# Performance work log

Hardware: AMD Instinct MI355X
Metric: run time of the kernel (lower is better)

## Reference

```python
import jax, jax.numpy as jnp
import numpy as np

DIM = 2048
STATE = 2048
SEL_H = 1024
B = 16384


def setup_inputs() -> dict:
    key = jax.random.key(0)
    ks = jax.random.split(key, 7)
    def lin(k, out_f, in_f):
        return jax.random.normal(k, (out_f, in_f), dtype=jnp.float32) / np.sqrt(in_f)
    return {
        "x_t": jax.random.normal(ks[0], (B, DIM), dtype=jnp.float32),
        "h_prev": jax.random.normal(ks[1], (B, STATE), dtype=jnp.float32),
        "W_in": lin(ks[2], STATE, DIM),
        "W_sel_in": lin(ks[3], SEL_H, DIM),
        "W_sel_out": lin(ks[4], 4 * STATE, SEL_H),
        "W_out": lin(ks[5], DIM, STATE),
        "d": jnp.ones((STATE,), dtype=jnp.float32),
    }


def reference(x_t, h_prev, W_in, W_sel_in, W_sel_out, W_out, d):
    # u_t = in_proj(x_t): [B, state]
    u_t = x_t @ W_in.T
    # selector: silu(x @ W_sel_in.T) @ W_sel_out.T -> [B, 4*state]
    sel_h = jax.nn.silu(x_t @ W_sel_in.T)
    sel = sel_h @ W_sel_out.T
    a_raw, b_raw, c_raw, d_raw = jnp.split(sel, 4, axis=-1)
    a_t = jax.nn.sigmoid(a_raw)
    b_t = jnp.tanh(b_raw)
    c_t = jnp.tanh(c_raw)
    d_t = jax.nn.sigmoid(d_raw)
    h_t = a_t * h_prev + b_t * u_t
    y_t = c_t * h_t + d[None, :] * d_t * u_t
    out = y_t @ W_out.T  # [B, dim]
    return (out, h_t)
```

## Files before the change

### kernel.cpp

```cpp
#include <hip/hip_runtime.h>
#include <hip/hip_bf16.h>
#include <cstdint>

#define NB    16384
#define DIMX  2048
#define STATE 2048
#define SELH  1024

typedef unsigned short u16;
typedef short  short8_t __attribute__((ext_vector_type(8)));
typedef float  f32x4    __attribute__((ext_vector_type(4)));

__device__ __forceinline__ u16 f2bf(float f) {
  unsigned u = __builtin_bit_cast(unsigned, f);
  u += 0x7fffu + ((u >> 16) & 1u);
  return (u16)(u >> 16);
}
__device__ __forceinline__ float bf2f(u16 h) {
  unsigned u = ((unsigned)h) << 16;
  return __builtin_bit_cast(float, u);
}
__device__ __forceinline__ float sigmoidf_(float x) { return 1.f / (1.f + __expf(-x)); }
__device__ __forceinline__ float tanhf_(float x)    { return 2.f / (1.f + __expf(-2.f * x)) - 1.f; }

__device__ __forceinline__ f32x4 mfma_bf16(short8_t a, short8_t b, f32x4 c) {
  return __builtin_amdgcn_mfma_f32_16x16x32_bf16(a, b, c, 0, 0, 0);
}

__device__ __forceinline__ void gload16(const void* g, const void* l) {
  __builtin_amdgcn_global_load_lds(
      (const __attribute__((address_space(1))) unsigned int*)(uintptr_t)g,
      (__attribute__((address_space(3))) unsigned int*)(unsigned int)(uintptr_t)l,
      16, 0, 0);
}

#define LDS_V(p) (*(const short8_t*)__builtin_assume_aligned((const void*)(p), 16))

__global__ __launch_bounds__(256) void k_f32_to_bf16(const float* __restrict__ src,
                                                     u16* __restrict__ dst, int n4) {
  int i = blockIdx.x * blockDim.x + threadIdx.x;
  int stride = gridDim.x * blockDim.x;
  for (; i < n4; i += stride) {
    float4 v = ((const float4*)src)[i];
    ushort4 o;
    o.x = f2bf(v.x); o.y = f2bf(v.y); o.z = f2bf(v.z); o.w = f2bf(v.w);
    ((ushort4*)dst)[i] = o;
  }
}

template <int EPI, int KD, int NCOLS>
__global__ __launch_bounds__(512, 2) void k_gemm256(const u16* __restrict__ A,
                                                    const u16* __restrict__ Bsrc,
                                                    float* __restrict__ f32out,
                                                    u16* __restrict__ bfout,
                                                    const float* __restrict__ hprev,
                                                    const u16* __restrict__ ubf,
                                                    const float* __restrict__ dvec) {
  __shared__ __align__(16) char smem[131072];
  const int tid = threadIdx.x;
  const int w = tid >> 6, l = tid & 63;
  const int wr = w >> 2, wc = w & 3;
  const int bx = blockIdx.x, by = blockIdx.y;
  const int m0 = by * 256;

  const unsigned aAddr0 = (unsigned)(wr * 16384 + (l & 15) * 128 +
                                     (((l >> 4) * 16) ^ ((l & 7) << 4)));
  const unsigned aAddr1 = aAddr0 ^ 64u;
  const unsigned bAddr0 = (unsigned)(65536 + (wc * 64 + (l & 15)) * 64 +
                                     (((l >> 4) * 16) ^ ((l & 3) << 4)));
  const unsigned bAddr1 = bAddr0 + 16384u;

  const int rA = tid >> 3;
  const int kA = ((tid & 7) ^ ((tid >> 3) & 7)) * 8;
  const u16* aSrc = A + (size_t)(m0 + rA) * KD + kA;

  const int rB = tid >> 2;
  const int kB = ((tid & 3) ^ ((tid >> 2) & 3)) * 8;
  size_t bRow0, bRow1;
  if constexpr (EPI <= 2) {
    bRow0 = (size_t)bx * 256 + rB;
    bRow1 = bRow0 + 128;
  } else {
    const int s0 = bx * 64;
    const int r1 = rB + 128;
    bRow0 = (size_t)((rB >> 4) & 3) * STATE + s0 + (rB >> 6) * 16 + (rB & 15);
    bRow1 = (size_t)((r1 >> 4) & 3) * STATE + s0 + (r1 >> 6) * 16 + (r1 & 15);
  }
  const u16* bSrc0 = Bsrc + bRow0 * KD + kB;
  const u16* bSrc1 = Bsrc + bRow1 * KD + kB;

  auto stageA = [&](int k0n, int rh, unsigned dstD) {
    const u16* sp = aSrc + (size_t)rh * 128 * KD + k0n;
    gload16(sp,           smem + dstD + (unsigned)rh * 16384u + (unsigned)tid * 16u);
    gload16(sp + 64 * KD, smem + dstD + (unsigned)rh * 16384u + 8192u + (unsigned)tid * 16u);
  };
  auto stageB = [&](int k0n, int kh, unsigned dstD) {
    const int kk = k0n + kh * 32;
    gload16(bSrc0 + kk, smem + 65536u + dstD + (unsigned)kh * 16384u + (unsigned)tid * 16u);
    gload16(bSrc1 + kk, smem + 65536u + dstD + (unsigned)kh * 16384u + 8192u + (unsigned)tid * 16u);
  };

  f32x4 acc[8][4];
#pragma unroll
  for (int i = 0; i < 8; ++i)
#pragma unroll
    for (int j = 0; j < 4; ++j) acc[i][j] = f32x4{0.f, 0.f, 0.f, 0.f};

  short8_t avq[4], bk0[4], bk1[4];

#define PH_TAIL()                                                              \
    __builtin_amdgcn_s_barrier();                                              \
    asm volatile("s_waitcnt lgkmcnt(0)" ::: "memory");                         \
    __builtin_amdgcn_sched_barrier(0);

#define MFMA16(MBASE, BK)                                                      \
    __builtin_amdgcn_s_setprio(1);                                             \
    _Pragma("unroll") for (int mf = 0; mf < 4; ++mf)                           \
      _Pragma("unroll") for (int nf = 0; nf < 4; ++nf)                         \
        acc[(MBASE) + mf][nf] = mfma_bf16(avq[mf], BK[nf],                     \
                                          acc[(MBASE) + mf][nf]);              \
    __builtin_amdgcn_s_setprio(0);                                             \
    __builtin_amdgcn_s_barrier();

#define KTILE(D, DO_STAGE, K0N, LASTT)                                         \
  {                                                                            \
                                                   \
    _Pragma("unroll") for (int mf = 0; mf < 4; ++mf)                           \
        avq[mf] = LDS_V(smem + aAddr0 + (D) * 32768u + mf * 2048u);            \
    _Pragma("unroll") for (int nf = 0; nf < 4; ++nf)                           \
        bk0[nf] = LDS_V(smem + bAddr0 + (D) * 32768u + nf * 1024u);            \
    if (DO_STAGE) stageA(K0N, 0, (D ^ 1) * 32768u);                            \
    PH_TAIL();                                                                 \
    MFMA16(0, bk0);                                                            \
                                                   \
    _Pragma("unroll") for (int mf = 0; mf < 4; ++mf)                           \
        avq[mf] = LDS_V(smem + aAddr0 + (D) * 32768u + (mf + 4) * 2048u);      \
    if (DO_STAGE) stageA(K0N, 1, (D ^ 1) * 32768u);                            \
    if (LASTT) { asm volatile("s_waitcnt vmcnt(0)" ::: "memory"); }            \
    else       { asm volatile("s_waitcnt vmcnt(4)" ::: "memory"); }            \
    PH_TAIL();                                                                 \
    MFMA16(4, bk0);                                                            \
                                                   \
    _Pragma("unroll") for (int mf = 0; mf < 4; ++mf)                           \
        avq[mf] = LDS_V(smem + aAddr1 + (D) * 32768u + mf * 2048u);            \
    _Pragma("unroll") for (int nf = 0; nf < 4; ++nf)                           \
        bk1[nf] = LDS_V(smem + bAddr1 + (D) * 32768u + nf * 1024u);            \
    if (DO_STAGE) stageB(K0N, 0, (D ^ 1) * 32768u);                            \
    PH_TAIL();                                                                 \
    MFMA16(0, bk1);                                                            \
                                                   \
    _Pragma("unroll") for (int mf = 0; mf < 4; ++mf)                           \
        avq[mf] = LDS_V(smem + aAddr1 + (D) * 32768u + (mf + 4) * 2048u);      \
    if (DO_STAGE) stageB(K0N, 1, (D ^ 1) * 32768u);                            \
    if (!LASTT) { asm volatile("s_waitcnt vmcnt(2)" ::: "memory"); }           \
    PH_TAIL();                                                                 \
    MFMA16(4, bk1);                                                            \
  }

  stageA(0, 0, 0u); stageA(0, 1, 0u); stageB(0, 0, 0u); stageB(0, 1, 0u);
  asm volatile("s_waitcnt vmcnt(2)" ::: "memory");
  __builtin_amdgcn_s_barrier();

  constexpr int NT = KD / 64;
  int k0 = 0;
#pragma unroll 1
  for (int T = 0; T < NT - 2; T += 2) {
    KTILE(0, true, k0 + 64, false);
    KTILE(1, true, k0 + 128, false);
    k0 += 128;
  }
  KTILE(0, true, k0 + 64, false);
  KTILE(1, false, 0, true);

#undef KTILE
#undef MFMA16
#undef PH_TAIL

  const int rbase = m0 + wr * 128 + ((l >> 4) << 2);
  if constexpr (EPI <= 2) {
    const int cbase = bx * 256 + wc * 64 + (l & 15);
#pragma unroll
    for (int mf = 0; mf < 8; ++mf)
#pragma unroll
      for (int nf = 0; nf < 4; ++nf)
#pragma unroll
        for (int r = 0; r < 4; ++r) {
          const int row = rbase + mf * 16 + r;
          const int col = cbase + nf * 16;
          const size_t idx = (size_t)row * NCOLS + col;
          const float v = acc[mf][nf][r];
          if constexpr (EPI == 0) {
            bfout[idx] = f2bf(v);
          } else if constexpr (EPI == 1) {
            bfout[idx] = f2bf(v * sigmoidf_(v));
          } else {
            f32out[idx] = v;
          }
        }
  } else {
    const int s = bx * 64 + wc * 16 + (l & 15);
    const float dval = dvec[s];
#pragma unroll
    for (int mf = 0; mf < 8; ++mf)
#pragma unroll
      for (int r = 0; r < 4; ++r) {
        const int row = rbase + mf * 16 + r;
        const size_t idx = (size_t)row * STATE + s;
        const float a  = acc[mf][0][r];
        const float b  = acc[mf][1][r];
        const float c  = acc[mf][2][r];
        const float dd = acc[mf][3][r];
        const float uu = bf2f(ubf[idx]);
        const float hp = hprev[idx];
        const float h = sigmoidf_(a) * hp + tanhf_(b) * uu;
        f32out[idx] = h;
        bfout[idx] = f2bf(tanhf_(c) * h + dval * sigmoidf_(dd) * uu);
      }
  }
}

extern "C" void kernel_launch(void* const* d_in, const int* in_sizes, int n_in,
                              void* d_out, int out_size, void* d_ws, size_t ws_size,
                              hipStream_t stream) {
  const float* x   = (const float*)d_in[0];
  const float* h0  = (const float*)d_in[1];
  const float* Win = (const float*)d_in[2];
  const float* Wsi = (const float*)d_in[3];
  const float* Wso = (const float*)d_in[4];
  const float* Wou = (const float*)d_in[5];
  const float* dv  = (const float*)d_in[6];
  float* out  = (float*)d_out;
  float* hout = out + (size_t)NB * DIMX;

  u16* ws = (u16*)d_ws;
  size_t o = 0;
  u16* xb   = ws + o; o += (size_t)NB * DIMX;
  u16* ub   = ws + o; o += (size_t)NB * STATE;
  u16* yb   = ws + o; o += (size_t)NB * STATE;
  u16* sh   = ws + o; o += (size_t)NB * SELH;
  u16* wib  = ws + o; o += (size_t)STATE * DIMX;
  u16* wsib = ws + o; o += (size_t)SELH * DIMX;
  u16* wsob = ws + o; o += (size_t)4 * STATE * SELH;
  u16* wob  = ws + o; o += (size_t)DIMX * STATE;

  k_f32_to_bf16<<<1024, 256, 0, stream>>>(x,   xb,   NB * DIMX / 4);
  k_f32_to_bf16<<<256,  256, 0, stream>>>(Win, wib,  STATE * DIMX / 4);
  k_f32_to_bf16<<<128,  256, 0, stream>>>(Wsi, wsib, SELH * DIMX / 4);
  k_f32_to_bf16<<<512,  256, 0, stream>>>(Wso, wsob, 4 * STATE * SELH / 4);
  k_f32_to_bf16<<<256,  256, 0, stream>>>(Wou, wob,  DIMX * STATE / 4);

  const dim3 blk(512);
  k_gemm256<0, DIMX, STATE><<<dim3(STATE / 256, NB / 256), blk, 0, stream>>>(
      xb, wib, nullptr, ub, nullptr, nullptr, nullptr);
  k_gemm256<1, DIMX, SELH><<<dim3(SELH / 256, NB / 256), blk, 0, stream>>>(
      xb, wsib, nullptr, sh, nullptr, nullptr, nullptr);
  k_gemm256<3, SELH, 0><<<dim3(STATE / 64, NB / 256), blk, 0, stream>>>(
      sh, wsob, hout, yb, h0, ub, dv);
  k_gemm256<2, STATE, DIMX><<<dim3(DIMX / 256, NB / 256), blk, 0, stream>>>(
      yb, wob, out, nullptr, nullptr, nullptr, nullptr);
}
```

Measured before the change: 800.2 us.

## Switch GEMM to 32x32x16 MFMA with simplified double-buffered pipeline

Replaces the 16x16x32 bf16 MFMA tiling with 32x32x16 MFMAs, reorganising the LDS layout, swizzle and per-wave fragment loads. The fine-grained four-phase schedule with partial vmcnt waits becomes one full wait and barrier per K tile, followed by staging the next tile. The gated epilogue now splits gates across wave pairs and passes h through an LDS stash between two syncthreads phases. Larger MFMAs cut LDS fragment traffic per flop, but the coarser synchronisation may expose global load latency and the epilogue adds extra barriers.

```diff
diff --git a/kernel.cpp b/kernel.cpp
--- a/kernel.cpp
+++ b/kernel.cpp
@@ -9,7 +9,7 @@
 
 typedef unsigned short u16;
 typedef short  short8_t __attribute__((ext_vector_type(8)));
-typedef float  f32x4    __attribute__((ext_vector_type(4)));
+typedef float  f32x16   __attribute__((ext_vector_type(16)));
 
 __device__ __forceinline__ u16 f2bf(float f) {
   unsigned u = __builtin_bit_cast(unsigned, f);
@@ -23,8 +23,8 @@
 __device__ __forceinline__ float sigmoidf_(float x) { return 1.f / (1.f + __expf(-x)); }
 __device__ __forceinline__ float tanhf_(float x)    { return 2.f / (1.f + __expf(-2.f * x)) - 1.f; }
 
-__device__ __forceinline__ f32x4 mfma_bf16(short8_t a, short8_t b, f32x4 c) {
-  return __builtin_amdgcn_mfma_f32_16x16x32_bf16(a, b, c, 0, 0, 0);
+__device__ __forceinline__ f32x16 mfma32(short8_t a, short8_t b, f32x16 c) {
+  return __builtin_amdgcn_mfma_f32_32x32x16_bf16(a, b, c, 0, 0, 0);
 }
 
 __device__ __forceinline__ void gload16(const void* g, const void* l) {
@@ -63,132 +63,90 @@
   const int bx = blockIdx.x, by = blockIdx.y;
   const int m0 = by * 256;
 
-  const unsigned aAddr0 = (unsigned)(wr * 16384 + (l & 15) * 128 +
-                                     (((l >> 4) * 16) ^ ((l & 7) << 4)));
-  const unsigned aAddr1 = aAddr0 ^ 64u;
-  const unsigned bAddr0 = (unsigned)(65536 + (wc * 64 + (l & 15)) * 64 +
-                                     (((l >> 4) * 16) ^ ((l & 3) << 4)));
-  const unsigned bAddr1 = bAddr0 + 16384u;
-
-  const int rA = tid >> 3;
-  const int kA = ((tid & 7) ^ ((tid >> 3) & 7)) * 8;
-  const u16* aSrc = A + (size_t)(m0 + rA) * KD + kA;
-
-  const int rB = tid >> 2;
-  const int kB = ((tid & 3) ^ ((tid >> 2) & 3)) * 8;
-  size_t bRow0, bRow1;
+  const unsigned x0 = (unsigned)(((l >> 5) * 16) ^ ((l & 7) << 4));
+  const unsigned kx[4] = {x0, x0 ^ 32u, x0 ^ 64u, x0 ^ 96u};
+  const unsigned aRowB = (unsigned)(wr * 16384 + (l & 31) * 128);
+  const unsigned bRowB = (unsigned)(wc * 8192 + (l & 31) * 128);
+
+  const int rT = tid >> 3;
+  const int kT = ((tid & 7) ^ (rT & 7)) * 8;
+  const u16* aSrc = A + (size_t)(m0 + rT) * KD + kT;
+  const u16* bSrcP[4];
+#pragma unroll
+  for (int g = 0; g < 4; ++g) {
+    const int r = g * 64 + rT;
+    size_t wrow;
+    if constexpr (EPI <= 2) {
+      wrow = (size_t)bx * 256 + r;
+    } else {
+      wrow = (size_t)((r >> 5) & 3) * STATE + bx * 64 + (r >> 7) * 32 + (r & 31);
+    }
+    bSrcP[g] = Bsrc + wrow * KD + kT;
+  }
+
+  auto stageAll = [&](int k0n, unsigned Dd) {
+#pragma unroll
+    for (int g = 0; g < 4; ++g)
+      gload16(aSrc + (size_t)g * 64 * KD + k0n,
+              smem + Dd * 32768u + g * 8192u + (unsigned)tid * 16u);
+#pragma unroll
+    for (int g = 0; g < 4; ++g)
+      gload16(bSrcP[g] + k0n,
+              smem + 65536u + Dd * 32768u + g * 8192u + (unsigned)tid * 16u);
+  };
+
+  f32x16 acc[4][2];
+#pragma unroll
+  for (int i = 0; i < 4; ++i)
+#pragma unroll
+    for (int j = 0; j < 2; ++j)
+#pragma unroll
+      for (int r = 0; r < 16; ++r) acc[i][j][r] = 0.f;
+
+#define KTILE(D, DO_STAGE, K0N)                                                \
+  {                                                                            \
+    asm volatile("s_waitcnt lgkmcnt(0)" ::: "memory");                         \
+    asm volatile("s_waitcnt vmcnt(0)" ::: "memory");                           \
+    __builtin_amdgcn_s_barrier();                                              \
+    __builtin_amdgcn_sched_barrier(0);                                         \
+    if (DO_STAGE) stageAll((K0N), (D) ^ 1u);                                   \
+    _Pragma("unroll") for (int kk = 0; kk < 4; ++kk) {                         \
+      short8_t af[4], bf[2];                                                   \
+      _Pragma("unroll") for (int mf = 0; mf < 4; ++mf)                         \
+          af[mf] = LDS_V(smem + (D) * 32768u + aRowB + mf * 4096u + kx[kk]);   \
+      _Pragma("unroll") for (int nf = 0; nf < 2; ++nf)                         \
+          bf[nf] = LDS_V(smem + 65536u + (D) * 32768u + bRowB + nf * 4096u +   \
+                         kx[kk]);                                              \
+      __builtin_amdgcn_s_setprio(1);                                           \
+      _Pragma("unroll") for (int mf = 0; mf < 4; ++mf)                         \
+        _Pragma("unroll") for (int nf = 0; nf < 2; ++nf)                       \
+            acc[mf][nf] = mfma32(af[mf], bf[nf], acc[mf][nf]);                 \
+      __builtin_amdgcn_s_setprio(0);                                           \
+    }                                                                          \
+  }
+
+  stageAll(0, 0u);
+
+  constexpr int NT = KD / 64;
+#pragma unroll 1
+  for (int T = 0; T < NT; T += 2) {
+    KTILE(0u, (T + 1 < NT), (T + 1) * 64);
+    KTILE(1u, (T + 2 < NT), (T + 2) * 64);
+  }
+#undef KTILE
+
   if constexpr (EPI <= 2) {
-    bRow0 = (size_t)bx * 256 + rB;
-    bRow1 = bRow0 + 128;
-  } else {
-    const int s0 = bx * 64;
-    const int r1 = rB + 128;
-    bRow0 = (size_t)((rB >> 4) & 3) * STATE + s0 + (rB >> 6) * 16 + (rB & 15);
-    bRow1 = (size_t)((r1 >> 4) & 3) * STATE + s0 + (r1 >> 6) * 16 + (r1 & 15);
-  }
-  const u16* bSrc0 = Bsrc + bRow0 * KD + kB;
-  const u16* bSrc1 = Bsrc + bRow1 * KD + kB;
-
-  auto stageA = [&](int k0n, int rh, unsigned dstD) {
-    const u16* sp = aSrc + (size_t)rh * 128 * KD + k0n;
-    gload16(sp,           smem + dstD + (unsigned)rh * 16384u + (unsigned)tid * 16u);
-    gload16(sp + 64 * KD, smem + dstD + (unsigned)rh * 16384u + 8192u + (unsigned)tid * 16u);
-  };
-  auto stageB = [&](int k0n, int kh, unsigned dstD) {
-    const int kk = k0n + kh * 32;
-    gload16(bSrc0 + kk, smem + 65536u + dstD + (unsigned)kh * 16384u + (unsigned)tid * 16u);
-    gload16(bSrc1 + kk, smem + 65536u + dstD + (unsigned)kh * 16384u + 8192u + (unsigned)tid * 16u);
-  };
-
-  f32x4 acc[8][4];
-#pragma unroll
-  for (int i = 0; i < 8; ++i)
-#pragma unroll
-    for (int j = 0; j < 4; ++j) acc[i][j] = f32x4{0.f, 0.f, 0.f, 0.f};
-
-  short8_t avq[4], bk0[4], bk1[4];
-
-#define PH_TAIL()                                                              \
-    __builtin_amdgcn_s_barrier();                                              \
-    asm volatile("s_waitcnt lgkmcnt(0)" ::: "memory");                         \
-    __builtin_amdgcn_sched_barrier(0);
-
-#define MFMA16(MBASE, BK)                                                      \
-    __builtin_amdgcn_s_setprio(1);                                             \
-    _Pragma("unroll") for (int mf = 0; mf < 4; ++mf)                           \
-      _Pragma("unroll") for (int nf = 0; nf < 4; ++nf)                         \
-        acc[(MBASE) + mf][nf] = mfma_bf16(avq[mf], BK[nf],                     \
-                                          acc[(MBASE) + mf][nf]);              \
-    __builtin_amdgcn_s_setprio(0);                                             \
-    __builtin_amdgcn_s_barrier();
-
-#define KTILE(D, DO_STAGE, K0N, LASTT)                                         \
-  {                                                                            \
-                                                   \
-    _Pragma("unroll") for (int mf = 0; mf < 4; ++mf)                           \
-        avq[mf] = LDS_V(smem + aAddr0 + (D) * 32768u + mf * 2048u);            \
-    _Pragma("unroll") for (int nf = 0; nf < 4; ++nf)                           \
-        bk0[nf] = LDS_V(smem + bAddr0 + (D) * 32768u + nf * 1024u);            \
-    if (DO_STAGE) stageA(K0N, 0, (D ^ 1) * 32768u);                            \
-    PH_TAIL();                                                                 \
-    MFMA16(0, bk0);                                                            \
-                                                   \
-    _Pragma("unroll") for (int mf = 0; mf < 4; ++mf)                           \
-        avq[mf] = LDS_V(smem + aAddr0 + (D) * 32768u + (mf + 4) * 2048u);      \
-    if (DO_STAGE) stageA(K0N, 1, (D ^ 1) * 32768u);                            \
-    if (LASTT) { asm volatile("s_waitcnt vmcnt(0)" ::: "memory"); }            \
-    else       { asm volatile("s_waitcnt vmcnt(4)" ::: "memory"); }            \
-    PH_TAIL();                                                                 \
-    MFMA16(4, bk0);                                                            \
-                                                   \
-    _Pragma("unroll") for (int mf = 0; mf < 4; ++mf)                           \
-        avq[mf] = LDS_V(smem + aAddr1 + (D) * 32768u + mf * 2048u);            \
-    _Pragma("unroll") for (int nf = 0; nf < 4; ++nf)                           \
-        bk1[nf] = LDS_V(smem + bAddr1 + (D) * 32768u + nf * 1024u);            \
-    if (DO_STAGE) stageB(K0N, 0, (D ^ 1) * 32768u);                            \
-    PH_TAIL();                                                                 \
-    MFMA16(0, bk1);                                                            \
-                                                   \
-    _Pragma("unroll") for (int mf = 0; mf < 4; ++mf)                           \
-        avq[mf] = LDS_V(smem + aAddr1 + (D) * 32768u + (mf + 4) * 2048u);      \
-    if (DO_STAGE) stageB(K0N, 1, (D ^ 1) * 32768u);                            \
-    if (!LASTT) { asm volatile("s_waitcnt vmcnt(2)" ::: "memory"); }           \
-    PH_TAIL();                                                                 \
-    MFMA16(4, bk1);                                                            \
-  }
-
-  stageA(0, 0, 0u); stageA(0, 1, 0u); stageB(0, 0, 0u); stageB(0, 1, 0u);
-  asm volatile("s_waitcnt vmcnt(2)" ::: "memory");
-  __builtin_amdgcn_s_barrier();
-
-  constexpr int NT = KD / 64;
-  int k0 = 0;
-#pragma unroll 1
-  for (int T = 0; T < NT - 2; T += 2) {
-    KTILE(0, true, k0 + 64, false);
-    KTILE(1, true, k0 + 128, false);
-    k0 += 128;
-  }
-  KTILE(0, true, k0 + 64, false);
-  KTILE(1, false, 0, true);
-
-#undef KTILE
-#undef MFMA16
-#undef PH_TAIL
-
-  const int rbase = m0 + wr * 128 + ((l >> 4) << 2);
-  if constexpr (EPI <= 2) {
-    const int cbase = bx * 256 + wc * 64 + (l & 15);
-#pragma unroll
-    for (int mf = 0; mf < 8; ++mf)
-#pragma unroll
-      for (int nf = 0; nf < 4; ++nf)
-#pragma unroll
-        for (int r = 0; r < 4; ++r) {
-          const int row = rbase + mf * 16 + r;
-          const int col = cbase + nf * 16;
+#pragma unroll
+    for (int mf = 0; mf < 4; ++mf)
+#pragma unroll
+      for (int nf = 0; nf < 2; ++nf)
+#pragma unroll
+        for (int reg = 0; reg < 16; ++reg) {
+          const int row = m0 + wr * 128 + mf * 32 +
+                          (reg & 3) + 8 * (reg >> 2) + 4 * (l >> 5);
+          const int col = bx * 256 + wc * 64 + nf * 32 + (l & 31);
           const size_t idx = (size_t)row * NCOLS + col;
-          const float v = acc[mf][nf][r];
+          const float v = acc[mf][nf][reg];
           if constexpr (EPI == 0) {
             bfout[idx] = f2bf(v);
           } else if constexpr (EPI == 1) {
@@ -198,24 +156,46 @@
           }
         }
   } else {
-    const int s = bx * 64 + wc * 16 + (l & 15);
-    const float dval = dvec[s];
-#pragma unroll
-    for (int mf = 0; mf < 8; ++mf)
-#pragma unroll
-      for (int r = 0; r < 4; ++r) {
-        const int row = rbase + mf * 16 + r;
-        const size_t idx = (size_t)row * STATE + s;
-        const float a  = acc[mf][0][r];
-        const float b  = acc[mf][1][r];
-        const float c  = acc[mf][2][r];
-        const float dd = acc[mf][3][r];
-        const float uu = bf2f(ubf[idx]);
-        const float hp = hprev[idx];
-        const float h = sigmoidf_(a) * hp + tanhf_(b) * uu;
-        f32out[idx] = h;
-        bfout[idx] = f2bf(tanhf_(c) * h + dval * sigmoidf_(dd) * uu);
-      }
+    const int t = wc >> 1;
+    const bool evenw = (wc & 1) == 0;
+    const int s = bx * 64 + t * 32 + (l & 31);
+    float* hstash = (float*)smem;
+    const int stashBase = (wr * 2 + t) * 128 * 33;
+    __syncthreads();
+    if (evenw) {
+#pragma unroll
+      for (int mf = 0; mf < 4; ++mf)
+#pragma unroll
+        for (int reg = 0; reg < 16; ++reg) {
+          const int lrow = mf * 32 + (reg & 3) + 8 * (reg >> 2) + 4 * (l >> 5);
+          const int row = m0 + wr * 128 + lrow;
+          const size_t idx = (size_t)row * STATE + s;
+          const float a = acc[mf][0][reg];
+          const float b = acc[mf][1][reg];
+          const float uu = bf2f(ubf[idx]);
+          const float hp = hprev[idx];
+          const float h = sigmoidf_(a) * hp + tanhf_(b) * uu;
+          f32out[idx] = h;
+          hstash[stashBase + lrow * 33 + (l & 31)] = h;
+        }
+    }
+    __syncthreads();
+    if (!evenw) {
+      const float dval = dvec[s];
+#pragma unroll
+      for (int mf = 0; mf < 4; ++mf)
+#pragma unroll
+        for (int reg = 0; reg < 16; ++reg) {
+          const int lrow = mf * 32 + (reg & 3) + 8 * (reg >> 2) + 4 * (l >> 5);
+          const int row = m0 + wr * 128 + lrow;
+          const size_t idx = (size_t)row * STATE + s;
+          const float c = acc[mf][0][reg];
+          const float dd = acc[mf][1][reg];
+          const float uu = bf2f(ubf[idx]);
+          const float h = hstash[stashBase + lrow * 33 + (l & 31)];
+          bfout[idx] = f2bf(tanhf_(c) * h + dval * sigmoidf_(dd) * uu);
+        }
+    }
   }
 }
 
```

Result: slower. 879.7 us (+9.9%).
